# Kernel optimization log

Hardware: AMD Instinct MI355X
Metric: run time of the kernel (lower is better)

The kernel has to match this reference:

```python
import jax, jax.numpy as jnp
import numpy as np

N_NODES = 50000
N_EDGES = 800000
LEAKY_SLOPE = 0.01
DROPOUT_P = 0.5


def _graph_conv(src, dst, x, W, b):
    """DGL GraphConv with norm='both': D_out^{-1/2} A D_in^{-1/2} X W + b."""
    n = x.shape[0]
    ones = jnp.ones((src.shape[0],), dtype=x.dtype)
    deg_out = jax.ops.segment_sum(ones, src, num_segments=n)  # out-degree of src nodes
    deg_in = jax.ops.segment_sum(ones, dst, num_segments=n)   # in-degree of dst nodes
    norm_src = jax.lax.rsqrt(jnp.maximum(deg_out, 1.0))
    norm_dst = jax.lax.rsqrt(jnp.maximum(deg_in, 1.0))
    h = (x * norm_src[:, None]) @ W          # apply weight before aggregation
    agg = jax.ops.segment_sum(h[src], dst, num_segments=n)  # SpMM aggregate
    return agg * norm_dst[:, None] + b


def _dropout(x, key, p=DROPOUT_P):
    keep = jax.random.bernoulli(key, 1.0 - p, x.shape)
    return jnp.where(keep, x / (1.0 - p), jnp.zeros((), x.dtype))


def setup_inputs() -> dict:
    key = jax.random.key(0)
    ks = jax.random.split(key, 8)
    features = jax.random.normal(ks[0], (N_NODES, 128), dtype=jnp.float32)
    src = jax.random.randint(ks[1], (N_EDGES,), 0, N_NODES, dtype=jnp.int64)
    dst = jax.random.randint(ks[2], (N_EDGES,), 0, N_NODES, dtype=jnp.int64)
    s1 = 1.0 / np.sqrt(128.0)
    s3 = 1.0 / np.sqrt(128.0)
    W1 = jax.random.normal(ks[3], (128, 128), dtype=jnp.float32) * s1
    W2 = jax.random.normal(ks[4], (128, 128), dtype=jnp.float32) * s1
    W3 = jax.random.normal(ks[5], (128, 64), dtype=jnp.float32) * s3
    b1 = jnp.zeros((128,), dtype=jnp.float32)
    b2 = jnp.zeros((128,), dtype=jnp.float32)
    b3 = jnp.zeros((64,), dtype=jnp.float32)
    return {"features": features, "src": src, "dst": dst,
            "W1": W1, "b1": b1, "W2": W2, "b2": b2, "W3": W3, "b3": b3}


def reference(features, src, dst, W1, b1, W2, b2, W3, b3):
    dk = jax.random.split(jax.random.key(42), 3)
    h = jax.nn.leaky_relu(_graph_conv(src, dst, features, W1, b1), LEAKY_SLOPE)
    h = _dropout(h, dk[0])
    h = jax.nn.leaky_relu(_graph_conv(src, dst, h, W2, b2), LEAKY_SLOPE)
    h = _dropout(h, dk[1])
    h = jax.nn.leaky_relu(_graph_conv(src, dst, h, W3, b3), LEAKY_SLOPE)
    h = _dropout(h, dk[2])
    return h
```

## Files before the change

kernel.cpp:

```cpp
#include <hip/hip_runtime.h>
#include <stdint.h>

using short8  = __attribute__((ext_vector_type(8))) short;
using f32x4   = __attribute__((ext_vector_type(4))) float;

#define TFR(r) { x0 += x1; x1 = (x1 << r) | (x1 >> (32 - r)); x1 ^= x0; }

__host__ __device__ inline void threefry2x32(uint32_t k0, uint32_t k1,
                                             uint32_t c0, uint32_t c1,
                                             uint32_t& o0, uint32_t& o1) {
  uint32_t ks2 = k0 ^ k1 ^ 0x1BD11BDAu;
  uint32_t x0 = c0 + k0, x1 = c1 + k1;
  TFR(13) TFR(15) TFR(26) TFR(6)  x0 += k1;  x1 += ks2 + 1u;
  TFR(17) TFR(29) TFR(16) TFR(24) x0 += ks2; x1 += k0 + 2u;
  TFR(13) TFR(15) TFR(26) TFR(6)  x0 += k0;  x1 += k1 + 3u;
  TFR(17) TFR(29) TFR(16) TFR(24) x0 += k1;  x1 += ks2 + 4u;
  TFR(13) TFR(15) TFR(26) TFR(6)  x0 += ks2; x1 += k0 + 5u;
  o0 = x0; o1 = x1;
}

__device__ inline float tf_uniform(uint32_t k0, uint32_t k1, uint32_t i) {
  uint32_t o0, o1;
  threefry2x32(k0, k1, 0u, i, o0, o1);
  uint32_t bits = o0 ^ o1;
  return __uint_as_float((bits >> 9) | 0x3F800000u) - 1.0f;
}

__device__ inline uint16_t f2bf(float f) {
  uint32_t u = __float_as_uint(f);
  return (uint16_t)((u + 0x7FFFu + ((u >> 16) & 1u)) >> 16);
}
__device__ inline uint32_t pack2bf(float a, float b) {
  return (uint32_t)f2bf(a) | ((uint32_t)f2bf(b) << 16);
}

#define SLOT_CAP 64

__global__ void fill_graph_kernel(const int* __restrict__ src, const int* __restrict__ dst,
                                  int* __restrict__ cursor, int* __restrict__ deg_out,
                                  uint16_t* __restrict__ edge_slots, int nE) {
  int e = blockIdx.x * blockDim.x + threadIdx.x;
  if (e >= nE) return;
  int s = src[e], d = dst[e];
  int pos = atomicAdd(&cursor[d], 1);
  if (pos < SLOT_CAP) edge_slots[(d << 6) + pos] = (uint16_t)s;
  atomicAdd(&deg_out[s], 1);
}

__global__ void convert_weights_kernel(const float* __restrict__ W1,
                                       const float* __restrict__ W2,
                                       const float* __restrict__ W3,
                                       uint16_t* __restrict__ Wt) {
  int i = blockIdx.x * 256 + (int)threadIdx.x;
  float v;
  if (i < 16384) {
    int nr = i >> 7, k = i & 127;
    v = W1[k * 128 + nr];
  } else if (i < 32768) {
    int j = i - 16384, nr = j >> 7, k = j & 127;
    v = W2[k * 128 + nr];
  } else if (i < 40960) {
    int j = i - 32768, nr = j >> 7, k = j & 127;
    v = W3[k * 64 + nr];
  } else return;
  Wt[i] = f2bf(v);
}

template<int COLS, bool IN_F32>
__global__ __launch_bounds__(256) void gemm_mfma(
    const void* __restrict__ Xin, const int* __restrict__ deg_out,
    const uint16_t* __restrict__ Wt, uint16_t* __restrict__ H, int n) {
  constexpr int LDW = 136;
  __shared__ uint16_t Xs[64 * LDW];
  __shared__ uint16_t Ws[COLS * LDW];
  __shared__ float ns[64];
  const int r0 = blockIdx.x * 64;
  const int tid = threadIdx.x;

  if (IN_F32) {
    const float* Xf = (const float*)Xin;
    for (int i = tid * 8; i < 64 * 128; i += 256 * 8) {
      int rl = i >> 7, col = i & 127, row = r0 + rl;
      uint4 w = make_uint4(0u, 0u, 0u, 0u);
      if (row < n) {
        float4 v0 = *(const float4*)&Xf[(size_t)row * 128 + col];
        float4 v1 = *(const float4*)&Xf[(size_t)row * 128 + col + 4];
        w.x = pack2bf(v0.x, v0.y); w.y = pack2bf(v0.z, v0.w);
        w.z = pack2bf(v1.x, v1.y); w.w = pack2bf(v1.z, v1.w);
      }
      *(uint4*)&Xs[rl * LDW + col] = w;
    }
  } else {
    const uint16_t* Xb = (const uint16_t*)Xin;
    for (int i = tid * 8; i < 64 * 128; i += 256 * 8) {
      int rl = i >> 7, col = i & 127, row = r0 + rl;
      uint4 w = make_uint4(0u, 0u, 0u, 0u);
      if (row < n) w = *(const uint4*)&Xb[(size_t)row * 128 + col];
      *(uint4*)&Xs[rl * LDW + col] = w;
    }
  }
  for (int i = tid * 8; i < COLS * 128; i += 256 * 8) {
    int nr = i >> 7, k = i & 127;
    *(uint4*)&Ws[nr * LDW + k] = *(const uint4*)&Wt[nr * 128 + k];
  }
  if (tid < 64) {
    int row = r0 + tid;
    int d = (row < n) ? deg_out[row] : 1;
    ns[tid] = rsqrtf(fmaxf((float)d, 1.0f));
  }
  __syncthreads();

  const int wave = tid >> 6, lane = tid & 63;
  const int wm = wave & 1, wn = wave >> 1;
  const int lane15 = lane & 15, quad = lane >> 4;
  constexpr int NT = COLS / 32;

  f32x4 acc[2][NT] = {};
  #pragma unroll
  for (int kc = 0; kc < 128; kc += 32) {
    short8 a0 = *(const short8*)&Xs[(wm * 32 + lane15) * LDW + kc + quad * 8];
    short8 a1 = *(const short8*)&Xs[(wm * 32 + 16 + lane15) * LDW + kc + quad * 8];
    #pragma unroll
    for (int nt = 0; nt < NT; ++nt) {
      int nn = wn * (COLS / 2) + nt * 16 + lane15;
      short8 b = *(const short8*)&Ws[nn * LDW + kc + quad * 8];
      acc[0][nt] = __builtin_amdgcn_mfma_f32_16x16x32_bf16(a0, b, acc[0][nt], 0, 0, 0);
      acc[1][nt] = __builtin_amdgcn_mfma_f32_16x16x32_bf16(a1, b, acc[1][nt], 0, 0, 0);
    }
  }

  #pragma unroll
  for (int mt = 0; mt < 2; ++mt) {
    #pragma unroll
    for (int nt = 0; nt < NT; ++nt) {
      #pragma unroll
      for (int reg = 0; reg < 4; ++reg) {
        int rl = wm * 32 + mt * 16 + quad * 4 + reg;
        int row = r0 + rl;
        if (row < n) {
          int col = wn * (COLS / 2) + nt * 16 + lane15;
          H[(size_t)row * COLS + col] = f2bf(acc[mt][nt][reg] * ns[rl]);
        }
      }
    }
  }
}

__device__ inline void accum8(float* acc, uint4 r) {
  acc[0] += __uint_as_float(r.x << 16);
  acc[1] += __uint_as_float(r.x & 0xFFFF0000u);
  acc[2] += __uint_as_float(r.y << 16);
  acc[3] += __uint_as_float(r.y & 0xFFFF0000u);
  acc[4] += __uint_as_float(r.z << 16);
  acc[5] += __uint_as_float(r.z & 0xFFFF0000u);
  acc[6] += __uint_as_float(r.w << 16);
  acc[7] += __uint_as_float(r.w & 0xFFFF0000u);
}

template<int COLS, bool OUT_BF16>
__global__ __launch_bounds__(256) void gather_fused(
    const uint16_t* __restrict__ h, const int* __restrict__ cursor,
    const uint16_t* __restrict__ edge_slots, const float* __restrict__ bias,
    void* __restrict__ outv, uint32_t k0, uint32_t k1, int n) {
  constexpr int TPN = COLS / 8;
  constexpr int NPB = 256 / TPN;
  const int node = blockIdx.x * NPB + (int)(threadIdx.x / TPN);
  if (node >= n) return;
  const int c8 = (threadIdx.x % TPN) * 8;

  const int deg = min(cursor[node], SLOT_CAP);
  const uint16_t* slots = edge_slots + ((size_t)node << 6);
  const uint16_t* hb = h + c8;
  float acc[8] = {0.f, 0.f, 0.f, 0.f, 0.f, 0.f, 0.f, 0.f};

  int e = 0;
  for (; e + 4 <= deg; e += 4) {
    int s0 = slots[e], s1 = slots[e + 1], s2 = slots[e + 2], s3 = slots[e + 3];
    uint4 r0 = *(const uint4*)(hb + (size_t)s0 * COLS);
    uint4 r1 = *(const uint4*)(hb + (size_t)s1 * COLS);
    uint4 r2 = *(const uint4*)(hb + (size_t)s2 * COLS);
    uint4 r3 = *(const uint4*)(hb + (size_t)s3 * COLS);
    accum8(acc, r0); accum8(acc, r1); accum8(acc, r2); accum8(acc, r3);
  }
  for (; e < deg; ++e) {
    uint4 r = *(const uint4*)(hb + (size_t)slots[e] * COLS);
    accum8(acc, r);
  }

  const float nd = rsqrtf(fmaxf((float)deg, 1.0f));
  const float4 b0 = *(const float4*)&bias[c8];
  const float4 b1 = *(const float4*)&bias[c8 + 4];
  const float bb[8] = {b0.x, b0.y, b0.z, b0.w, b1.x, b1.y, b1.z, b1.w};
  const uint32_t i0 = (uint32_t)(node * COLS + c8);

  float o[8];
  #pragma unroll
  for (int j = 0; j < 8; ++j) {
    float v = acc[j] * nd + bb[j];
    v = (v >= 0.f) ? v : 0.01f * v;
    o[j] = (tf_uniform(k0, k1, i0 + (uint32_t)j) < 0.5f) ? v * 2.0f : 0.0f;
  }

  if (OUT_BF16) {
    uint16_t* out = (uint16_t*)outv;
    uint4 w;
    w.x = pack2bf(o[0], o[1]); w.y = pack2bf(o[2], o[3]);
    w.z = pack2bf(o[4], o[5]); w.w = pack2bf(o[6], o[7]);
    *(uint4*)&out[(size_t)node * COLS + c8] = w;
  } else {
    float* out = (float*)outv;
    float* op = &out[(size_t)node * COLS + c8];
    *(float4*)op = make_float4(o[0], o[1], o[2], o[3]);
    *(float4*)(op + 4) = make_float4(o[4], o[5], o[6], o[7]);
  }
}

extern "C" void kernel_launch(void* const* d_in, const int* in_sizes, int n_in,
                              void* d_out, int out_size, void* d_ws, size_t ws_size,
                              hipStream_t stream) {
  const float* features = (const float*)d_in[0];
  const int*   src      = (const int*)d_in[1];
  const int*   dst      = (const int*)d_in[2];
  const float* W1       = (const float*)d_in[3];
  const float* b1       = (const float*)d_in[4];
  const float* W2       = (const float*)d_in[5];
  const float* b2       = (const float*)d_in[6];
  const float* W3       = (const float*)d_in[7];
  const float* b3       = (const float*)d_in[8];
  float* out = (float*)d_out;

  const int n  = in_sizes[0] / 128;
  const int nE = in_sizes[1];

  char* p = (char*)d_ws;
  int* deg_out        = (int*)p;      p += (size_t)n * 4;
  int* cursor         = (int*)p;      p += (size_t)n * 4;
  uint16_t* edge_slots = (uint16_t*)p; p += (size_t)n * SLOT_CAP * 2;
  uint16_t* Wt        = (uint16_t*)p; p += 40960 * 2;
  uint16_t* h         = (uint16_t*)p; p += (size_t)n * 128 * 2;
  uint16_t* xb        = (uint16_t*)p;

  uint32_t dk[3][2];
  for (uint32_t i = 0; i < 3; ++i)
    threefry2x32(0u, 42u, 0u, i, dk[i][0], dk[i][1]);

  const int eb = (nE + 255) / 256;

  hipMemsetAsync(deg_out, 0, (size_t)2 * n * sizeof(int), stream);
  convert_weights_kernel<<<160, 256, 0, stream>>>(W1, W2, W3, Wt);
  fill_graph_kernel<<<eb, 256, 0, stream>>>(src, dst, cursor, deg_out, edge_slots, nE);

  const int gb = (n + 63) / 64;
  const int g128 = (n + 15) / 16;
  const int g64  = (n + 31) / 32;

  gemm_mfma<128, true><<<gb, 256, 0, stream>>>(features, deg_out, Wt, h, n);
  gather_fused<128, true><<<g128, 256, 0, stream>>>(h, cursor, edge_slots, b1, xb,
                                                    dk[0][0], dk[0][1], n);
  gemm_mfma<128, false><<<gb, 256, 0, stream>>>(xb, deg_out, Wt + 16384, h, n);
  gather_fused<128, true><<<g128, 256, 0, stream>>>(h, cursor, edge_slots, b2, xb,
                                                    dk[1][0], dk[1][1], n);
  gemm_mfma<64, false><<<gb, 256, 0, stream>>>(xb, deg_out, Wt + 32768, h, n);
  gather_fused<64, false><<<g64, 256, 0, stream>>>(h, cursor, edge_slots, b3, out,
                                                   dk[2][0], dk[2][1], n);
}
```

Measured before the change: 292.4 us.

## Fuse graph build with first GEMM and gather with following GEMM per layer

Measured after the change: 322.6 us. +10.3%, slower.

```diff
diff --git a/kernel.cpp b/kernel.cpp
--- a/kernel.cpp
+++ b/kernel.cpp
@@ -1,8 +1,11 @@
 #include <hip/hip_runtime.h>
 #include <stdint.h>
 
-using short8  = __attribute__((ext_vector_type(8))) short;
-using f32x4   = __attribute__((ext_vector_type(4))) float;
+using short8 = __attribute__((ext_vector_type(8))) short;
+using f32x4  = __attribute__((ext_vector_type(4))) float;
+
+#define SLOT_CAP 64
+#define LDW 136
 
 #define TFR(r) { x0 += x1; x1 = (x1 << r) | (x1 >> (32 - r)); x1 ^= x0; }
 
@@ -33,19 +36,8 @@
 __device__ inline uint32_t pack2bf(float a, float b) {
   return (uint32_t)f2bf(a) | ((uint32_t)f2bf(b) << 16);
 }
-
-#define SLOT_CAP 64
-
-__global__ void fill_graph_kernel(const int* __restrict__ src, const int* __restrict__ dst,
-                                  int* __restrict__ cursor, int* __restrict__ deg_out,
-                                  uint16_t* __restrict__ edge_slots, int nE) {
-  int e = blockIdx.x * blockDim.x + threadIdx.x;
-  if (e >= nE) return;
-  int s = src[e], d = dst[e];
-  int pos = atomicAdd(&cursor[d], 1);
-  if (pos < SLOT_CAP) edge_slots[(d << 6) + pos] = (uint16_t)s;
-  atomicAdd(&deg_out[s], 1);
-}
+__device__ inline float bflo(uint32_t w) { return __uint_as_float(w << 16); }
+__device__ inline float bfhi(uint32_t w) { return __uint_as_float(w & 0xFFFF0000u); }
 
 __global__ void convert_weights_kernel(const float* __restrict__ W1,
                                        const float* __restrict__ W2,
@@ -66,50 +58,16 @@
   Wt[i] = f2bf(v);
 }
 
-template<int COLS, bool IN_F32>
-__global__ __launch_bounds__(256) void gemm_mfma(
-    const void* __restrict__ Xin, const int* __restrict__ deg_out,
-    const uint16_t* __restrict__ Wt, uint16_t* __restrict__ H, int n) {
-  constexpr int LDW = 136;
-  __shared__ uint16_t Xs[64 * LDW];
-  __shared__ uint16_t Ws[COLS * LDW];
-  __shared__ float ns[64];
-  const int r0 = blockIdx.x * 64;
-  const int tid = threadIdx.x;
-
-  if (IN_F32) {
-    const float* Xf = (const float*)Xin;
-    for (int i = tid * 8; i < 64 * 128; i += 256 * 8) {
-      int rl = i >> 7, col = i & 127, row = r0 + rl;
-      uint4 w = make_uint4(0u, 0u, 0u, 0u);
-      if (row < n) {
-        float4 v0 = *(const float4*)&Xf[(size_t)row * 128 + col];
-        float4 v1 = *(const float4*)&Xf[(size_t)row * 128 + col + 4];
-        w.x = pack2bf(v0.x, v0.y); w.y = pack2bf(v0.z, v0.w);
-        w.z = pack2bf(v1.x, v1.y); w.w = pack2bf(v1.z, v1.w);
-      }
-      *(uint4*)&Xs[rl * LDW + col] = w;
-    }
-  } else {
-    const uint16_t* Xb = (const uint16_t*)Xin;
-    for (int i = tid * 8; i < 64 * 128; i += 256 * 8) {
-      int rl = i >> 7, col = i & 127, row = r0 + rl;
-      uint4 w = make_uint4(0u, 0u, 0u, 0u);
-      if (row < n) w = *(const uint4*)&Xb[(size_t)row * 128 + col];
-      *(uint4*)&Xs[rl * LDW + col] = w;
-    }
-  }
-  for (int i = tid * 8; i < COLS * 128; i += 256 * 8) {
-    int nr = i >> 7, k = i & 127;
-    *(uint4*)&Ws[nr * LDW + k] = *(const uint4*)&Wt[nr * 128 + k];
-  }
-  if (tid < 64) {
-    int row = r0 + tid;
-    int d = (row < n) ? deg_out[row] : 1;
-    ns[tid] = rsqrtf(fmaxf((float)d, 1.0f));
-  }
-  __syncthreads();
-
+__global__ void norms_kernel(const int* __restrict__ deg_out,
+                             float* __restrict__ nsrc, int n) {
+  int v = blockIdx.x * 256 + (int)threadIdx.x;
+  if (v < n) nsrc[v] = rsqrtf(fmaxf((float)deg_out[v], 1.0f));
+}
+
+template<int COLS, bool SCALE>
+__device__ inline void mfma_phase_store(const uint16_t* Xs, const uint16_t* Ws,
+                                        const float* ns_s, uint16_t* H,
+                                        int r0, int n, int tid) {
   const int wave = tid >> 6, lane = tid & 63;
   const int wm = wave & 1, wn = wave >> 1;
   const int lane15 = lane & 15, quad = lane >> 4;
@@ -122,8 +80,7 @@
     short8 a1 = *(const short8*)&Xs[(wm * 32 + 16 + lane15) * LDW + kc + quad * 8];
     #pragma unroll
     for (int nt = 0; nt < NT; ++nt) {
-      int nn = wn * (COLS / 2) + nt * 16 + lane15;
-      short8 b = *(const short8*)&Ws[nn * LDW + kc + quad * 8];
+      short8 b = *(const short8*)&Ws[(wn * (COLS / 2) + nt * 16 + lane15) * LDW + kc + quad * 8];
       acc[0][nt] = __builtin_amdgcn_mfma_f32_16x16x32_bf16(a0, b, acc[0][nt], 0, 0, 0);
       acc[1][nt] = __builtin_amdgcn_mfma_f32_16x16x32_bf16(a1, b, acc[1][nt], 0, 0, 0);
     }
@@ -139,59 +96,184 @@
         int row = r0 + rl;
         if (row < n) {
           int col = wn * (COLS / 2) + nt * 16 + lane15;
-          H[(size_t)row * COLS + col] = f2bf(acc[mt][nt][reg] * ns[rl]);
+          float v = acc[mt][nt][reg];
+          if (SCALE) v *= ns_s[rl];
+          H[(size_t)row * COLS + col] = f2bf(v);
         }
       }
     }
   }
 }
 
-__device__ inline void accum8(float* acc, uint4 r) {
-  acc[0] += __uint_as_float(r.x << 16);
-  acc[1] += __uint_as_float(r.x & 0xFFFF0000u);
-  acc[2] += __uint_as_float(r.y << 16);
-  acc[3] += __uint_as_float(r.y & 0xFFFF0000u);
-  acc[4] += __uint_as_float(r.z << 16);
-  acc[5] += __uint_as_float(r.z & 0xFFFF0000u);
-  acc[6] += __uint_as_float(r.w << 16);
-  acc[7] += __uint_as_float(r.w & 0xFFFF0000u);
-}
-
-template<int COLS, bool OUT_BF16>
-__global__ __launch_bounds__(256) void gather_fused(
-    const uint16_t* __restrict__ h, const int* __restrict__ cursor,
+__global__ __launch_bounds__(256) void mega1_kernel(
+    const int* __restrict__ src, const int* __restrict__ dst,
+    int* __restrict__ cursor, int* __restrict__ deg_out,
+    uint16_t* __restrict__ edge_slots,
+    const float* __restrict__ X, const uint16_t* __restrict__ Wt1,
+    uint16_t* __restrict__ h1, int n, int nE, int fillB) {
+  __shared__ uint16_t Xs[64 * LDW];
+  __shared__ uint16_t Ws[128 * LDW];
+
+  if ((int)blockIdx.x < fillB) {
+    int e = blockIdx.x * 256 + (int)threadIdx.x;
+    if (e < nE) {
+      int s = src[e], d = dst[e];
+      int pos = atomicAdd(&cursor[d], 1);
+      if (pos < SLOT_CAP) edge_slots[(d << 6) + pos] = (uint16_t)s;
+      atomicAdd(&deg_out[s], 1);
+    }
+    return;
+  }
+
+  const int r0 = ((int)blockIdx.x - fillB) * 64;
+  const int tid = threadIdx.x;
+
+  for (int i = tid * 8; i < 64 * 128; i += 256 * 8) {
+    int rl = i >> 7, col = i & 127, row = r0 + rl;
+    uint4 w = make_uint4(0u, 0u, 0u, 0u);
+    if (row < n) {
+      float4 v0 = *(const float4*)&X[(size_t)row * 128 + col];
+      float4 v1 = *(const float4*)&X[(size_t)row * 128 + col + 4];
+      w.x = pack2bf(v0.x, v0.y); w.y = pack2bf(v0.z, v0.w);
+      w.z = pack2bf(v1.x, v1.y); w.w = pack2bf(v1.z, v1.w);
+    }
+    *(uint4*)&Xs[rl * LDW + col] = w;
+  }
+  for (int i = tid * 8; i < 128 * 128; i += 256 * 8) {
+    int nr = i >> 7, k = i & 127;
+    *(uint4*)&Ws[nr * LDW + k] = *(const uint4*)&Wt1[nr * 128 + k];
+  }
+  __syncthreads();
+  mfma_phase_store<128, false>(Xs, Ws, nullptr, h1, r0, n, tid);
+}
+
+template<int NCOLS, bool PEN>
+__global__ __launch_bounds__(256) void fuse_gather_gemm_kernel(
+    const uint16_t* __restrict__ h_in, const int* __restrict__ cursor,
+    const uint16_t* __restrict__ edge_slots, const float* __restrict__ nsrc,
+    const float* __restrict__ bias, const uint16_t* __restrict__ Wt,
+    uint16_t* __restrict__ h_out, uint32_t k0, uint32_t k1, int n) {
+  __shared__ uint16_t Xs[64 * LDW];
+  __shared__ uint16_t Ws[NCOLS * LDW];
+  __shared__ float ns_s[64];
+  const int r0 = blockIdx.x * 64;
+  const int tid = threadIdx.x;
+
+  for (int i = tid * 8; i < NCOLS * 128; i += 256 * 8) {
+    int nr = i >> 7, k = i & 127;
+    *(uint4*)&Ws[nr * LDW + k] = *(const uint4*)&Wt[nr * 128 + k];
+  }
+  if (tid < 64) {
+    int row = r0 + tid;
+    ns_s[tid] = (row < n) ? nsrc[row] : 1.0f;
+  }
+
+  #pragma unroll
+  for (int it = 0; it < 2; ++it) {
+    const int nl = it * 32 + tid / 8;
+    const int node = r0 + nl;
+    const int c16 = (tid & 7) * 16;
+
+    if (node < n) {
+      float acc[16];
+      #pragma unroll
+      for (int j = 0; j < 16; ++j) acc[j] = 0.f;
+
+      const int dgi = cursor[node];
+      const int deg = min(dgi, SLOT_CAP);
+      const uint16_t* slots = edge_slots + ((size_t)node << 6);
+      const uint16_t* hb = h_in + c16;
+
+      #pragma unroll 2
+      for (int e = 0; e < deg; ++e) {
+        int s = slots[e];
+        const uint16_t* hr = hb + (size_t)s * 128;
+        uint4 ra = *(const uint4*)hr;
+        uint4 rb = *(const uint4*)(hr + 8);
+        if (PEN) {
+          float w = nsrc[s];
+          acc[0]  = fmaf(w, bflo(ra.x), acc[0]);  acc[1]  = fmaf(w, bfhi(ra.x), acc[1]);
+          acc[2]  = fmaf(w, bflo(ra.y), acc[2]);  acc[3]  = fmaf(w, bfhi(ra.y), acc[3]);
+          acc[4]  = fmaf(w, bflo(ra.z), acc[4]);  acc[5]  = fmaf(w, bfhi(ra.z), acc[5]);
+          acc[6]  = fmaf(w, bflo(ra.w), acc[6]);  acc[7]  = fmaf(w, bfhi(ra.w), acc[7]);
+          acc[8]  = fmaf(w, bflo(rb.x), acc[8]);  acc[9]  = fmaf(w, bfhi(rb.x), acc[9]);
+          acc[10] = fmaf(w, bflo(rb.y), acc[10]); acc[11] = fmaf(w, bfhi(rb.y), acc[11]);
+          acc[12] = fmaf(w, bflo(rb.z), acc[12]); acc[13] = fmaf(w, bfhi(rb.z), acc[13]);
+          acc[14] = fmaf(w, bflo(rb.w), acc[14]); acc[15] = fmaf(w, bfhi(rb.w), acc[15]);
+        } else {
+          acc[0]  += bflo(ra.x); acc[1]  += bfhi(ra.x);
+          acc[2]  += bflo(ra.y); acc[3]  += bfhi(ra.y);
+          acc[4]  += bflo(ra.z); acc[5]  += bfhi(ra.z);
+          acc[6]  += bflo(ra.w); acc[7]  += bfhi(ra.w);
+          acc[8]  += bflo(rb.x); acc[9]  += bfhi(rb.x);
+          acc[10] += bflo(rb.y); acc[11] += bfhi(rb.y);
+          acc[12] += bflo(rb.z); acc[13] += bfhi(rb.z);
+          acc[14] += bflo(rb.w); acc[15] += bfhi(rb.w);
+        }
+      }
+
+      const float nd = rsqrtf(fmaxf((float)dgi, 1.0f));
+      const float4 b0 = *(const float4*)&bias[c16];
+      const float4 b1 = *(const float4*)&bias[c16 + 4];
+      const float4 b2 = *(const float4*)&bias[c16 + 8];
+      const float4 b3 = *(const float4*)&bias[c16 + 12];
+      const float bb[16] = {b0.x, b0.y, b0.z, b0.w, b1.x, b1.y, b1.z, b1.w,
+                            b2.x, b2.y, b2.z, b2.w, b3.x, b3.y, b3.z, b3.w};
+      const uint32_t i0 = (uint32_t)(node * 128 + c16);
+
+      float o[16];
+      #pragma unroll
+      for (int j = 0; j < 16; ++j) {
+        float v = acc[j] * nd + bb[j];
+        v = (v >= 0.f) ? v : 0.01f * v;
+        o[j] = (tf_uniform(k0, k1, i0 + (uint32_t)j) < 0.5f) ? v * 2.0f : 0.0f;
+      }
+
+      uint4 w0, w1;
+      w0.x = pack2bf(o[0], o[1]);   w0.y = pack2bf(o[2], o[3]);
+      w0.z = pack2bf(o[4], o[5]);   w0.w = pack2bf(o[6], o[7]);
+      w1.x = pack2bf(o[8], o[9]);   w1.y = pack2bf(o[10], o[11]);
+      w1.z = pack2bf(o[12], o[13]); w1.w = pack2bf(o[14], o[15]);
+      *(uint4*)&Xs[nl * LDW + c16] = w0;
+      *(uint4*)&Xs[nl * LDW + c16 + 8] = w1;
+    } else {
+      uint4 z = make_uint4(0u, 0u, 0u, 0u);
+      *(uint4*)&Xs[nl * LDW + c16] = z;
+      *(uint4*)&Xs[nl * LDW + c16 + 8] = z;
+    }
+  }
+  __syncthreads();
+  mfma_phase_store<NCOLS, true>(Xs, Ws, ns_s, h_out, r0, n, tid);
+}
+
+__global__ __launch_bounds__(256) void gather_out_kernel(
+    const uint16_t* __restrict__ h3, const int* __restrict__ cursor,
     const uint16_t* __restrict__ edge_slots, const float* __restrict__ bias,
-    void* __restrict__ outv, uint32_t k0, uint32_t k1, int n) {
-  constexpr int TPN = COLS / 8;
-  constexpr int NPB = 256 / TPN;
-  const int node = blockIdx.x * NPB + (int)(threadIdx.x / TPN);
+    float* __restrict__ out, uint32_t k0, uint32_t k1, int n) {
+  const int node = blockIdx.x * 32 + (int)(threadIdx.x >> 3);
   if (node >= n) return;
-  const int c8 = (threadIdx.x % TPN) * 8;
-
-  const int deg = min(cursor[node], SLOT_CAP);
+  const int c8 = (threadIdx.x & 7) * 8;
+
+  const int dgi = cursor[node];
+  const int deg = min(dgi, SLOT_CAP);
   const uint16_t* slots = edge_slots + ((size_t)node << 6);
-  const uint16_t* hb = h + c8;
+  const uint16_t* hb = h3 + c8;
+
   float acc[8] = {0.f, 0.f, 0.f, 0.f, 0.f, 0.f, 0.f, 0.f};
-
-  int e = 0;
-  for (; e + 4 <= deg; e += 4) {
-    int s0 = slots[e], s1 = slots[e + 1], s2 = slots[e + 2], s3 = slots[e + 3];
-    uint4 r0 = *(const uint4*)(hb + (size_t)s0 * COLS);
-    uint4 r1 = *(const uint4*)(hb + (size_t)s1 * COLS);
-    uint4 r2 = *(const uint4*)(hb + (size_t)s2 * COLS);
-    uint4 r3 = *(const uint4*)(hb + (size_t)s3 * COLS);
-    accum8(acc, r0); accum8(acc, r1); accum8(acc, r2); accum8(acc, r3);
-  }
-  for (; e < deg; ++e) {
-    uint4 r = *(const uint4*)(hb + (size_t)slots[e] * COLS);
-    accum8(acc, r);
-  }
-
-  const float nd = rsqrtf(fmaxf((float)deg, 1.0f));
+  #pragma unroll 2
+  for (int e = 0; e < deg; ++e) {
+    uint4 r = *(const uint4*)(hb + (size_t)slots[e] * 64);
+    acc[0] += bflo(r.x); acc[1] += bfhi(r.x);
+    acc[2] += bflo(r.y); acc[3] += bfhi(r.y);
+    acc[4] += bflo(r.z); acc[5] += bfhi(r.z);
+    acc[6] += bflo(r.w); acc[7] += bfhi(r.w);
+  }
+
+  const float nd = rsqrtf(fmaxf((float)dgi, 1.0f));
   const float4 b0 = *(const float4*)&bias[c8];
   const float4 b1 = *(const float4*)&bias[c8 + 4];
   const float bb[8] = {b0.x, b0.y, b0.z, b0.w, b1.x, b1.y, b1.z, b1.w};
-  const uint32_t i0 = (uint32_t)(node * COLS + c8);
+  const uint32_t i0 = (uint32_t)(node * 64 + c8);
 
   float o[8];
   #pragma unroll
@@ -201,18 +283,9 @@
     o[j] = (tf_uniform(k0, k1, i0 + (uint32_t)j) < 0.5f) ? v * 2.0f : 0.0f;
   }
 
-  if (OUT_BF16) {
-    uint16_t* out = (uint16_t*)outv;
-    uint4 w;
-    w.x = pack2bf(o[0], o[1]); w.y = pack2bf(o[2], o[3]);
-    w.z = pack2bf(o[4], o[5]); w.w = pack2bf(o[6], o[7]);
-    *(uint4*)&out[(size_t)node * COLS + c8] = w;
-  } else {
-    float* out = (float*)outv;
-    float* op = &out[(size_t)node * COLS + c8];
-    *(float4*)op = make_float4(o[0], o[1], o[2], o[3]);
-    *(float4*)(op + 4) = make_float4(o[4], o[5], o[6], o[7]);
-  }
+  float* op = &out[(size_t)node * 64 + c8];
+  *(float4*)op = make_float4(o[0], o[1], o[2], o[3]);
+  *(float4*)(op + 4) = make_float4(o[4], o[5], o[6], o[7]);
 }
 
 extern "C" void kernel_launch(void* const* d_in, const int* in_sizes, int n_in,
@@ -233,34 +306,31 @@
   const int nE = in_sizes[1];
 
   char* p = (char*)d_ws;
-  int* deg_out        = (int*)p;      p += (size_t)n * 4;
-  int* cursor         = (int*)p;      p += (size_t)n * 4;
+  int* deg_out         = (int*)p;      p += (size_t)n * 4;
+  int* cursor          = (int*)p;      p += (size_t)n * 4;
   uint16_t* edge_slots = (uint16_t*)p; p += (size_t)n * SLOT_CAP * 2;
-  uint16_t* Wt        = (uint16_t*)p; p += 40960 * 2;
-  uint16_t* h         = (uint16_t*)p; p += (size_t)n * 128 * 2;
-  uint16_t* xb        = (uint16_t*)p;
+  uint16_t* Wt         = (uint16_t*)p; p += 40960 * 2;
+  float* nsrc          = (float*)p;    p += (size_t)n * 4;
+  uint16_t* h1         = (uint16_t*)p; p += (size_t)n * 128 * 2;
+  uint16_t* h2         = (uint16_t*)p; p += (size_t)n * 128 * 2;
+  uint16_t* h3         = (uint16_t*)p;
 
   uint32_t dk[3][2];
   for (uint32_t i = 0; i < 3; ++i)
     threefry2x32(0u, 42u, 0u, i, dk[i][0], dk[i][1]);
 
-  const int eb = (nE + 255) / 256;
+  const int fillB = (nE + 255) / 256;
+  const int gb    = (n + 63) / 64;
 
   hipMemsetAsync(deg_out, 0, (size_t)2 * n * sizeof(int), stream);
   convert_weights_kernel<<<160, 256, 0, stream>>>(W1, W2, W3, Wt);
-  fill_graph_kernel<<<eb, 256, 0, stream>>>(src, dst, cursor, deg_out, edge_slots, nE);
-
-  const int gb = (n + 63) / 64;
-  const int g128 = (n + 15) / 16;
-  const int g64  = (n + 31) / 32;
-
-  gemm_mfma<128, true><<<gb, 256, 0, stream>>>(features, deg_out, Wt, h, n);
-  gather_fused<128, true><<<g128, 256, 0, stream>>>(h, cursor, edge_slots, b1, xb,
-                                                    dk[0][0], dk[0][1], n);
-  gemm_mfma<128, false><<<gb, 256, 0, stream>>>(xb, deg_out, Wt + 16384, h, n);
-  gather_fused<128, true><<<g128, 256, 0, stream>>>(h, cursor, edge_slots, b2, xb,
-                                                    dk[1][0], dk[1][1], n);
-  gemm_mfma<64, false><<<gb, 256, 0, stream>>>(xb, deg_out, Wt + 32768, h, n);
-  gather_fused<64, false><<<g64, 256, 0, stream>>>(h, cursor, edge_slots, b3, out,
-                                                   dk[2][0], dk[2][1], n);
-}
+  mega1_kernel<<<fillB + gb, 256, 0, stream>>>(src, dst, cursor, deg_out, edge_slots,
+                                               features, Wt, h1, n, nE, fillB);
+  norms_kernel<<<(n + 255) / 256, 256, 0, stream>>>(deg_out, nsrc, n);
+  fuse_gather_gemm_kernel<128, true><<<gb, 256, 0, stream>>>(
+      h1, cursor, edge_slots, nsrc, b1, Wt + 16384, h2, dk[0][0], dk[0][1], n);
+  fuse_gather_gemm_kernel<64, false><<<gb, 256, 0, stream>>>(
+      h2, cursor, edge_slots, nsrc, b2, Wt + 32768, h3, dk[1][0], dk[1][1], n);
+  gather_out_kernel<<<(n + 31) / 32, 256, 0, stream>>>(
+      h3, cursor, edge_slots, b3, out, dk[2][0], dk[2][1], n);
+}
```
